# Kernel optimization log

Hardware: AMD Instinct MI355X
Metric: run time of the kernel (lower is better)

## Reference

```python
import jax, jax.numpy as jnp
import numpy as np

DIM = 1024
EPS = 1e-12  # torch F.normalize eps


def setup_inputs() -> dict:
    key = jax.random.key(0)
    k1, k2, k3 = jax.random.split(key, 3)
    b, n, d = 2, 4096, DIM
    x = jax.random.normal(k1, (b, n, d), dtype=jnp.float32)
    # nn.Linear(dim, 3*dim, bias=False): weight shape [3*dim, dim]
    w_qkva = jax.random.normal(k2, (3 * d, d), dtype=jnp.float32) * (1.0 / np.sqrt(d))
    gamma = jnp.ones((d,), dtype=jnp.float32)  # RMSNorm gamma (init ones)
    return {"x": x, "gamma": gamma, "w_qkva": w_qkva}


def _rmsnorm(x, gamma):
    # lucidrains RMSNorm: F.normalize(x, dim=-1) * sqrt(dim) * gamma
    norm = jnp.sqrt(jnp.sum(x * x, axis=-1, keepdims=True))
    scale = jnp.asarray(np.sqrt(x.shape[-1]), x.dtype)
    return x / jnp.maximum(norm, EPS) * scale * gamma


def reference(x, gamma, w_qkva):
    d = x.shape[-1]
    xn = _rmsnorm(x, gamma)
    qkva = jnp.einsum('bnd,ed->bne', xn, w_qkva)  # [b, n, 3d]
    q, kv, a = qkva[..., :d], qkva[..., d:2 * d], qkva[..., 2 * d:]
    a = jax.nn.sigmoid(a)

    def binary_operator(e_i, e_j):
        a_i, kv_i = e_i
        a_j, kv_j = e_j
        return a_j * a_i, a_j * kv_i + kv_j

    # per-channel scalar linear recurrence: kv_t = a_t * kv_{t-1} + kv_t
    _, kv_scan = jax.lax.associative_scan(binary_operator, (a, kv), axis=1)
    return q * kv_scan  # [b, n, d]
```

## Files before the change

### kernel.cpp

```cpp
#include <hip/hip_runtime.h>
#include <cstdint>
#include <cstddef>

#define DIMD 1024
#define BB 2
#define NN 4096
#define MM (BB*NN)
#define EE (3*DIMD)
#define KK DIMD

typedef __attribute__((ext_vector_type(8))) short short8;
typedef __attribute__((ext_vector_type(4))) float f32x4;

__device__ __forceinline__ unsigned short f2bf(float f) {
  unsigned int u = __float_as_uint(f);
  u += 0x7FFF + ((u >> 16) & 1);
  return (unsigned short)(u >> 16);
}

#define GLOAD_LDS16(gptr, lptr) \
  __builtin_amdgcn_global_load_lds((const __attribute__((address_space(1))) void*)(gptr), \
                                   (__attribute__((address_space(3))) void*)(lptr), 16, 0, 0)

__global__ void cast_w_kernel(const float* __restrict__ w, unsigned short* __restrict__ wb) {
  int i = blockIdx.x * blockDim.x + threadIdx.x;
  const float4* w4 = (const float4*)w;
  float4 v = w4[i];
  unsigned int lo = (unsigned int)f2bf(v.x) | ((unsigned int)f2bf(v.y) << 16);
  unsigned int hi = (unsigned int)f2bf(v.z) | ((unsigned int)f2bf(v.w) << 16);
  ((uint2*)wb)[i] = make_uint2(lo, hi);
}

__global__ void rmsnorm_kernel(const float* __restrict__ x, const float* __restrict__ gamma,
                               unsigned short* __restrict__ xn) {
  int row = blockIdx.x;
  int tid = threadIdx.x;
  const float4* x4 = (const float4*)(x + (size_t)row * DIMD);
  float4 v = x4[tid];
  float ss = v.x*v.x + v.y*v.y + v.z*v.z + v.w*v.w;
  #pragma unroll
  for (int m = 32; m >= 1; m >>= 1) ss += __shfl_xor(ss, m);
  __shared__ float red[4];
  if ((tid & 63) == 0) red[tid >> 6] = ss;
  __syncthreads();
  float tot = red[0] + red[1] + red[2] + red[3];
  float scale = 32.0f / fmaxf(sqrtf(tot), 1e-12f);
  const float4* g4 = (const float4*)gamma;
  float4 g = g4[tid];
  float a0 = v.x*scale*g.x, a1 = v.y*scale*g.y, a2 = v.z*scale*g.z, a3 = v.w*scale*g.w;
  unsigned int lo = (unsigned int)f2bf(a0) | ((unsigned int)f2bf(a1) << 16);
  unsigned int hi = (unsigned int)f2bf(a2) | ((unsigned int)f2bf(a3) << 16);
  ((uint2*)(xn + (size_t)row * DIMD))[tid] = make_uint2(lo, hi);
}

#define BM 128
#define BN 128
#define BK 64

__global__ __launch_bounds__(256) void gemm_kernel(const unsigned short* __restrict__ A,
                                                   const unsigned short* __restrict__ Bw,
                                                   float* __restrict__ C) {
  __shared__ unsigned short Al[BM][BK];
  __shared__ unsigned short Bl[BN][BK];
  int tid = threadIdx.x;
  int l = tid & 63;
  int w = tid >> 6;
  int wr = w >> 1, wc = w & 1;
  int m0 = blockIdx.y * BM;
  int n0 = blockIdx.x * BN;
  int lrow = l & 15, lk = l >> 4;

  int srow_base = w * 32 + (l >> 3);
  int scol = (((l & 7) ^ (l >> 3)) * 8);

  f32x4 acc[4][4];
  #pragma unroll
  for (int i = 0; i < 4; i++)
    #pragma unroll
    for (int j = 0; j < 4; j++) acc[i][j] = (f32x4)(0.f);

  for (int k0 = 0; k0 < KK; k0 += BK) {
    __syncthreads();
    #pragma unroll
    for (int t = 0; t < 4; t++) {
      int row = srow_base + t * 8;
      GLOAD_LDS16(A  + (size_t)(m0 + row) * KK + k0 + scol, &Al[w*32 + t*8][0]);
      GLOAD_LDS16(Bw + (size_t)(n0 + row) * KK + k0 + scol, &Bl[w*32 + t*8][0]);
    }
    __syncthreads();
    #pragma unroll
    for (int s = 0; s < 2; s++) {
      short8 af[4], bf[4];
      #pragma unroll
      for (int i = 0; i < 4; i++) {
        int r = wr*64 + i*16 + lrow;
        af[i] = *(const short8*)&Al[r][((s*4 + lk) ^ (r & 7)) * 8];
      }
      #pragma unroll
      for (int j = 0; j < 4; j++) {
        int r = wc*64 + j*16 + lrow;
        bf[j] = *(const short8*)&Bl[r][((s*4 + lk) ^ (r & 7)) * 8];
      }
      #pragma unroll
      for (int i = 0; i < 4; i++)
        #pragma unroll
        for (int j = 0; j < 4; j++)
          acc[i][j] = __builtin_amdgcn_mfma_f32_16x16x32_bf16(af[i], bf[j], acc[i][j], 0, 0, 0);
    }
  }

  #pragma unroll
  for (int i = 0; i < 4; i++) {
    int rowb = m0 + wr*64 + i*16 + lk*4;
    #pragma unroll
    for (int j = 0; j < 4; j++) {
      int col = n0 + wc*64 + j*16 + lrow;
      f32x4 v = acc[i][j];
      bool isg = (col >= 2*DIMD);
      #pragma unroll
      for (int r = 0; r < 4; r++) {
        float val = v[r];
        if (isg) val = 1.0f / (1.0f + __expf(-val));
        C[(size_t)(rowb + r)*EE + col] = val;
      }
    }
  }
}

#define CHUNK 32
#define NCH (NN / CHUNK)

__global__ void scan1_kernel(const float* __restrict__ qkva,
                             float* __restrict__ Aagg, float* __restrict__ Kagg) {
  int d = threadIdx.x * 4;
  int c = blockIdx.x;
  int b = blockIdx.y;
  const float* p = qkva + ((size_t)(b*NN + c*CHUNK)) * EE;
  float4 Aa = make_float4(1.f,1.f,1.f,1.f);
  float4 Kv = make_float4(0.f,0.f,0.f,0.f);
  for (int i0 = 0; i0 < CHUNK; i0 += 4) {
    float4 av[4], kvv[4];
    #pragma unroll
    for (int u = 0; u < 4; u++) av[u]  = *(const float4*)&p[(size_t)(i0+u)*EE + 2*DIMD + d];
    #pragma unroll
    for (int u = 0; u < 4; u++) kvv[u] = *(const float4*)&p[(size_t)(i0+u)*EE + DIMD + d];
    #pragma unroll
    for (int u = 0; u < 4; u++) {
      Kv.x = fmaf(av[u].x, Kv.x, kvv[u].x); Aa.x *= av[u].x;
      Kv.y = fmaf(av[u].y, Kv.y, kvv[u].y); Aa.y *= av[u].y;
      Kv.z = fmaf(av[u].z, Kv.z, kvv[u].z); Aa.z *= av[u].z;
      Kv.w = fmaf(av[u].w, Kv.w, kvv[u].w); Aa.w *= av[u].w;
    }
  }
  size_t idx = (size_t)(b*NCH + c)*DIMD + d;
  *(float4*)&Aagg[idx] = Aa;
  *(float4*)&Kagg[idx] = Kv;
}

__global__ void scan2_kernel(const float* __restrict__ Aagg, const float* __restrict__ Kagg,
                             float* __restrict__ carry) {
  int t = blockIdx.x * 256 + threadIdx.x;
  int b = t >> 10, d = t & (DIMD - 1);
  float cy = 0.f;
  for (int c0 = 0; c0 < NCH; c0 += 8) {
    float Av[8], Kv[8];
    #pragma unroll
    for (int u = 0; u < 8; u++) {
      size_t idx = (size_t)(b*NCH + c0 + u)*DIMD + d;
      Av[u] = Aagg[idx]; Kv[u] = Kagg[idx];
    }
    #pragma unroll
    for (int u = 0; u < 8; u++) {
      carry[(size_t)(b*NCH + c0 + u)*DIMD + d] = cy;
      cy = fmaf(Av[u], cy, Kv[u]);
    }
  }
}

__global__ void scan3_kernel(const float* __restrict__ qkva, const float* __restrict__ carry,
                             float* __restrict__ out) {
  int d = threadIdx.x * 4;
  int c = blockIdx.x;
  int b = blockIdx.y;
  const float* p = qkva + ((size_t)(b*NN + c*CHUNK)) * EE;
  float* o = out + ((size_t)(b*NN + c*CHUNK)) * DIMD;
  float4 Kv = *(const float4*)&carry[(size_t)(b*NCH + c)*DIMD + d];
  for (int i0 = 0; i0 < CHUNK; i0 += 4) {
    float4 av[4], kvv[4], qv[4];
    #pragma unroll
    for (int u = 0; u < 4; u++) av[u]  = *(const float4*)&p[(size_t)(i0+u)*EE + 2*DIMD + d];
    #pragma unroll
    for (int u = 0; u < 4; u++) kvv[u] = *(const float4*)&p[(size_t)(i0+u)*EE + DIMD + d];
    #pragma unroll
    for (int u = 0; u < 4; u++) qv[u]  = *(const float4*)&p[(size_t)(i0+u)*EE + d];
    #pragma unroll
    for (int u = 0; u < 4; u++) {
      float4 r;
      Kv.x = fmaf(av[u].x, Kv.x, kvv[u].x); r.x = qv[u].x * Kv.x;
      Kv.y = fmaf(av[u].y, Kv.y, kvv[u].y); r.y = qv[u].y * Kv.y;
      Kv.z = fmaf(av[u].z, Kv.z, kvv[u].z); r.z = qv[u].z * Kv.z;
      Kv.w = fmaf(av[u].w, Kv.w, kvv[u].w); r.w = qv[u].w * Kv.w;
      *(float4*)&o[(size_t)(i0+u)*DIMD + d] = r;
    }
  }
}

extern "C" void kernel_launch(void* const* d_in, const int* in_sizes, int n_in,
                              void* d_out, int out_size, void* d_ws, size_t ws_size,
                              hipStream_t stream) {
  const float* x     = (const float*)d_in[0];
  const float* gamma = (const float*)d_in[1];
  const float* wq    = (const float*)d_in[2];
  float* out = (float*)d_out;
  char* ws = (char*)d_ws;

  unsigned short* Wb = (unsigned short*)ws;
  unsigned short* Xn = (unsigned short*)(ws + 6291456);
  float* qkva        = (float*)(ws + 23068672);
  float* Aagg        = (float*)(ws + 123731968);
  float* Kagg        = (float*)(ws + 124780544);
  float* carry       = (float*)(ws + 125829120);

  cast_w_kernel<<<(EE*KK)/(256*4), 256, 0, stream>>>(wq, Wb);
  rmsnorm_kernel<<<MM, 256, 0, stream>>>(x, gamma, Xn);
  gemm_kernel<<<dim3(EE/BN, MM/BM), 256, 0, stream>>>(Xn, Wb, qkva);
  scan1_kernel<<<dim3(NCH, BB), 256, 0, stream>>>(qkva, Aagg, Kagg);
  scan2_kernel<<<dim3((BB*DIMD)/256), 256, 0, stream>>>(Aagg, Kagg, carry);
  scan3_kernel<<<dim3(NCH, BB), 256, 0, stream>>>(qkva, carry, out);
}
```

Baseline: 204.4 us.

## Double-buffer GEMM LDS tiles and write q/kv/a as separate planes

The GEMM main loop now uses two LDS buffers. The next K-tile is issued with global_load_lds while MFMAs run on the current tile, so each iteration needs only one barrier instead of two. The GEMM epilogue also writes q, kv and the sigmoid gate into three contiguous [M,1024] planes instead of one interleaved [M,3072] buffer. The scan kernels read these planes with a stride of 1024, which is meant to improve locality for the scan passes. LDS use per block doubles to 64KB, which may limit how many blocks fit on each CU.

```diff
diff --git a/kernel.cpp b/kernel.cpp
--- a/kernel.cpp
+++ b/kernel.cpp
@@ -56,12 +56,15 @@
 #define BM 128
 #define BN 128
 #define BK 64
+#define NT (KK/BK)
 
 __global__ __launch_bounds__(256) void gemm_kernel(const unsigned short* __restrict__ A,
                                                    const unsigned short* __restrict__ Bw,
-                                                   float* __restrict__ C) {
-  __shared__ unsigned short Al[BM][BK];
-  __shared__ unsigned short Bl[BN][BK];
+                                                   float* __restrict__ q_pl,
+                                                   float* __restrict__ kv_pl,
+                                                   float* __restrict__ a_pl) {
+  __shared__ unsigned short Al[2][BM][BK];
+  __shared__ unsigned short Bl[2][BN][BK];
   int tid = threadIdx.x;
   int l = tid & 63;
   int w = tid >> 6;
@@ -70,8 +73,10 @@
   int n0 = blockIdx.x * BN;
   int lrow = l & 15, lk = l >> 4;
 
-  int srow_base = w * 32 + (l >> 3);
+  int srow = w * 32 + (l >> 3);
   int scol = (((l & 7) ^ (l >> 3)) * 8);
+  const unsigned short* Ag = A  + (size_t)(m0 + srow) * KK + scol;
+  const unsigned short* Bg = Bw + (size_t)(n0 + srow) * KK + scol;
 
   f32x4 acc[4][4];
   #pragma unroll
@@ -79,27 +84,35 @@
     #pragma unroll
     for (int j = 0; j < 4; j++) acc[i][j] = (f32x4)(0.f);
 
-  for (int k0 = 0; k0 < KK; k0 += BK) {
-    __syncthreads();
-    #pragma unroll
-    for (int t = 0; t < 4; t++) {
-      int row = srow_base + t * 8;
-      GLOAD_LDS16(A  + (size_t)(m0 + row) * KK + k0 + scol, &Al[w*32 + t*8][0]);
-      GLOAD_LDS16(Bw + (size_t)(n0 + row) * KK + k0 + scol, &Bl[w*32 + t*8][0]);
-    }
-    __syncthreads();
+  #pragma unroll
+  for (int t = 0; t < 4; t++) {
+    GLOAD_LDS16(Ag + (size_t)(t*8) * KK, &Al[0][w*32 + t*8][0]);
+    GLOAD_LDS16(Bg + (size_t)(t*8) * KK, &Bl[0][w*32 + t*8][0]);
+  }
+  __syncthreads();
+
+  int cur = 0;
+  for (int kt = 0; kt < NT; ++kt) {
+    if (kt + 1 < NT) {
+      int nk = (kt + 1) * BK;
+      #pragma unroll
+      for (int t = 0; t < 4; t++) {
+        GLOAD_LDS16(Ag + (size_t)(t*8) * KK + nk, &Al[cur ^ 1][w*32 + t*8][0]);
+        GLOAD_LDS16(Bg + (size_t)(t*8) * KK + nk, &Bl[cur ^ 1][w*32 + t*8][0]);
+      }
+    }
     #pragma unroll
     for (int s = 0; s < 2; s++) {
       short8 af[4], bf[4];
       #pragma unroll
       for (int i = 0; i < 4; i++) {
         int r = wr*64 + i*16 + lrow;
-        af[i] = *(const short8*)&Al[r][((s*4 + lk) ^ (r & 7)) * 8];
+        af[i] = *(const short8*)&Al[cur][r][((s*4 + lk) ^ (r & 7)) * 8];
       }
       #pragma unroll
       for (int j = 0; j < 4; j++) {
         int r = wc*64 + j*16 + lrow;
-        bf[j] = *(const short8*)&Bl[r][((s*4 + lk) ^ (r & 7)) * 8];
+        bf[j] = *(const short8*)&Bl[cur][r][((s*4 + lk) ^ (r & 7)) * 8];
       }
       #pragma unroll
       for (int i = 0; i < 4; i++)
@@ -107,21 +120,28 @@
         for (int j = 0; j < 4; j++)
           acc[i][j] = __builtin_amdgcn_mfma_f32_16x16x32_bf16(af[i], bf[j], acc[i][j], 0, 0, 0);
     }
-  }
-
+    if (kt + 1 < NT) {
+      __syncthreads();
+      cur ^= 1;
+    }
+  }
+
+  int plane = n0 >> 10;
+  float* P = (plane == 0) ? q_pl : ((plane == 1) ? kv_pl : a_pl);
+  bool isg = (plane == 2);
+  int pn0 = n0 & 1023;
   #pragma unroll
   for (int i = 0; i < 4; i++) {
     int rowb = m0 + wr*64 + i*16 + lk*4;
     #pragma unroll
     for (int j = 0; j < 4; j++) {
-      int col = n0 + wc*64 + j*16 + lrow;
+      int pcol = pn0 + wc*64 + j*16 + lrow;
       f32x4 v = acc[i][j];
-      bool isg = (col >= 2*DIMD);
       #pragma unroll
       for (int r = 0; r < 4; r++) {
         float val = v[r];
         if (isg) val = 1.0f / (1.0f + __expf(-val));
-        C[(size_t)(rowb + r)*EE + col] = val;
+        P[(size_t)(rowb + r)*DIMD + pcol] = val;
       }
     }
   }
@@ -130,20 +150,22 @@
 #define CHUNK 32
 #define NCH (NN / CHUNK)
 
-__global__ void scan1_kernel(const float* __restrict__ qkva,
+__global__ void scan1_kernel(const float* __restrict__ kv_pl, const float* __restrict__ a_pl,
                              float* __restrict__ Aagg, float* __restrict__ Kagg) {
   int d = threadIdx.x * 4;
   int c = blockIdx.x;
   int b = blockIdx.y;
-  const float* p = qkva + ((size_t)(b*NN + c*CHUNK)) * EE;
+  size_t base = ((size_t)(b*NN + c*CHUNK)) * DIMD + d;
+  const float* pa = a_pl + base;
+  const float* pk = kv_pl + base;
   float4 Aa = make_float4(1.f,1.f,1.f,1.f);
   float4 Kv = make_float4(0.f,0.f,0.f,0.f);
   for (int i0 = 0; i0 < CHUNK; i0 += 4) {
     float4 av[4], kvv[4];
     #pragma unroll
-    for (int u = 0; u < 4; u++) av[u]  = *(const float4*)&p[(size_t)(i0+u)*EE + 2*DIMD + d];
-    #pragma unroll
-    for (int u = 0; u < 4; u++) kvv[u] = *(const float4*)&p[(size_t)(i0+u)*EE + DIMD + d];
+    for (int u = 0; u < 4; u++) av[u]  = *(const float4*)&pa[(size_t)(i0+u)*DIMD];
+    #pragma unroll
+    for (int u = 0; u < 4; u++) kvv[u] = *(const float4*)&pk[(size_t)(i0+u)*DIMD];
     #pragma unroll
     for (int u = 0; u < 4; u++) {
       Kv.x = fmaf(av[u].x, Kv.x, kvv[u].x); Aa.x *= av[u].x;
@@ -177,22 +199,26 @@
   }
 }
 
-__global__ void scan3_kernel(const float* __restrict__ qkva, const float* __restrict__ carry,
+__global__ void scan3_kernel(const float* __restrict__ q_pl, const float* __restrict__ kv_pl,
+                             const float* __restrict__ a_pl, const float* __restrict__ carry,
                              float* __restrict__ out) {
   int d = threadIdx.x * 4;
   int c = blockIdx.x;
   int b = blockIdx.y;
-  const float* p = qkva + ((size_t)(b*NN + c*CHUNK)) * EE;
-  float* o = out + ((size_t)(b*NN + c*CHUNK)) * DIMD;
+  size_t base = ((size_t)(b*NN + c*CHUNK)) * DIMD + d;
+  const float* pa = a_pl + base;
+  const float* pk = kv_pl + base;
+  const float* pq = q_pl + base;
+  float* o = out + base;
   float4 Kv = *(const float4*)&carry[(size_t)(b*NCH + c)*DIMD + d];
   for (int i0 = 0; i0 < CHUNK; i0 += 4) {
     float4 av[4], kvv[4], qv[4];
     #pragma unroll
-    for (int u = 0; u < 4; u++) av[u]  = *(const float4*)&p[(size_t)(i0+u)*EE + 2*DIMD + d];
-    #pragma unroll
-    for (int u = 0; u < 4; u++) kvv[u] = *(const float4*)&p[(size_t)(i0+u)*EE + DIMD + d];
-    #pragma unroll
-    for (int u = 0; u < 4; u++) qv[u]  = *(const float4*)&p[(size_t)(i0+u)*EE + d];
+    for (int u = 0; u < 4; u++) av[u]  = *(const float4*)&pa[(size_t)(i0+u)*DIMD];
+    #pragma unroll
+    for (int u = 0; u < 4; u++) kvv[u] = *(const float4*)&pk[(size_t)(i0+u)*DIMD];
+    #pragma unroll
+    for (int u = 0; u < 4; u++) qv[u]  = *(const float4*)&pq[(size_t)(i0+u)*DIMD];
     #pragma unroll
     for (int u = 0; u < 4; u++) {
       float4 r;
@@ -200,7 +226,7 @@
       Kv.y = fmaf(av[u].y, Kv.y, kvv[u].y); r.y = qv[u].y * Kv.y;
       Kv.z = fmaf(av[u].z, Kv.z, kvv[u].z); r.z = qv[u].z * Kv.z;
       Kv.w = fmaf(av[u].w, Kv.w, kvv[u].w); r.w = qv[u].w * Kv.w;
-      *(float4*)&o[(size_t)(i0+u)*DIMD + d] = r;
+      *(float4*)&o[(size_t)(i0+u)*DIMD] = r;
     }
   }
 }
@@ -216,15 +242,17 @@
 
   unsigned short* Wb = (unsigned short*)ws;
   unsigned short* Xn = (unsigned short*)(ws + 6291456);
-  float* qkva        = (float*)(ws + 23068672);
+  float* q_pl        = (float*)(ws + 23068672);
+  float* kv_pl       = (float*)(ws + 56623104);
+  float* a_pl        = (float*)(ws + 90177536);
   float* Aagg        = (float*)(ws + 123731968);
   float* Kagg        = (float*)(ws + 124780544);
   float* carry       = (float*)(ws + 125829120);
 
   cast_w_kernel<<<(EE*KK)/(256*4), 256, 0, stream>>>(wq, Wb);
   rmsnorm_kernel<<<MM, 256, 0, stream>>>(x, gamma, Xn);
-  gemm_kernel<<<dim3(EE/BN, MM/BM), 256, 0, stream>>>(Xn, Wb, qkva);
-  scan1_kernel<<<dim3(NCH, BB), 256, 0, stream>>>(qkva, Aagg, Kagg);
+  gemm_kernel<<<dim3(EE/BN, MM/BM), 256, 0, stream>>>(Xn, Wb, q_pl, kv_pl, a_pl);
+  scan1_kernel<<<dim3(NCH, BB), 256, 0, stream>>>(kv_pl, a_pl, Aagg, Kagg);
   scan2_kernel<<<dim3((BB*DIMD)/256), 256, 0, stream>>>(Aagg, Kagg, carry);
-  scan3_kernel<<<dim3(NCH, BB), 256, 0, stream>>>(qkva, carry, out);
-}
+  scan3_kernel<<<dim3(NCH, BB), 256, 0, stream>>>(q_pl, kv_pl, a_pl, carry, out);
+}
```

Measured after the change: 201.5 us. No clear change (-1.5%).
